# Kernel tuning notes

Hardware: AMD Instinct MI355X
Metric: run time of the kernel (lower is better)

The kernel has to match this reference:

```python
import jax, jax.numpy as jnp
import numpy as np

CHEB_K = 2  # hops per support; stacked terms = 1 + 2*CHEB_K = 5


def setup_inputs() -> dict:
    key = jax.random.key(0)
    k1, k2, k3, k4, k5 = jax.random.split(key, 5)
    B, N, C, O, D = 16, 1024, 64, 64, 10
    return {
        "x": jax.random.normal(k1, (B, N, C), dtype=jnp.float32),
        "adj": jax.random.uniform(k2, (2, B, N, N), dtype=jnp.float32),
        "node_embedding": jax.random.normal(k3, (N, D), dtype=jnp.float32),
        "weights_pool": jax.random.normal(k4, (D, 2 * CHEB_K + 1, C, O), dtype=jnp.float32) * 0.1,
        "bias_pool": jax.random.normal(k5, (D, O), dtype=jnp.float32) * 0.1,
    }


def reference(x, adj, node_embedding, weights_pool, bias_pool):
    # k-hop graph aggregation over each of the 2 supports
    out = [x]
    for s in range(adj.shape[0]):
        a = adj[s]  # [B, N, N]
        x1 = x
        for _ in range(CHEB_K):
            x1 = jnp.einsum('bnm,bmc->bnc', a, x1)
            out.append(x1)
    x_g = jnp.stack(out, axis=2)  # [B, N, K, C] with K = 2*cheb_k+1 (already node-major)
    # per-node hypernetwork weights and bias from node embeddings
    weights = jnp.einsum('nd,dkio->nkio', node_embedding, weights_pool)  # [N, K, C, O]
    bias = node_embedding @ bias_pool  # [N, O]
    # per-node contraction over (K, C)
    return jnp.einsum('bnki,nkio->bno', x_g, weights) + bias
```

## Files before the change

### kernel.cpp

```cpp
#include <hip/hip_runtime.h>
#include <stdint.h>


typedef __attribute__((ext_vector_type(4))) float f32x4;
typedef __attribute__((ext_vector_type(2))) float f32x2;
typedef __attribute__((ext_vector_type(8))) short s16x8;
typedef __attribute__((ext_vector_type(8))) __bf16 bf16x8;

__device__ __forceinline__ unsigned short f2bf(float f) {
  union { float f; uint32_t u; } v; v.f = f;
  uint32_t r = v.u + 0x7FFFu + ((v.u >> 16) & 1u);
  return (unsigned short)(r >> 16);
}
__device__ __forceinline__ uint32_t pack2(float a, float b) {
  return (uint32_t)f2bf(a) | ((uint32_t)f2bf(b) << 16);
}

union FragU { s16x8 s; bf16x8 b; uint32_t u[4]; };

__device__ __forceinline__ void async_cp16(const void* g, void* l) {
  __builtin_amdgcn_global_load_lds(
      (const __attribute__((address_space(1))) void*)g,
      (__attribute__((address_space(3))) void*)l, 16, 0, 0);
}

__global__ __launch_bounds__(256) void prep(const float* __restrict__ x,
                                            const float* __restrict__ wp,
                                            unsigned short* __restrict__ XT0,
                                            unsigned short* __restrict__ wpTb) {
  __shared__ __align__(16) char smem[17160];
  const int tid = threadIdx.x;
  const int bid = blockIdx.x;
  if (bid < 256) {
    unsigned short (*tl)[72] = (unsigned short(*)[72])smem;
    const int b = bid >> 4, n0 = (bid & 15) * 64;
    {
      const int c4 = (tid & 15) * 4;
#pragma unroll
      for (int i = 0; i < 4; ++i) {
        const int row = (tid >> 4) + i * 16;
        f32x4 v =
            *(const f32x4*)(x + ((size_t)(b * 1024 + n0 + row)) * 64 + c4);
        *(uint32_t*)&tl[row][c4]     = pack2(v[0], v[1]);
        *(uint32_t*)&tl[row][c4 + 2] = pack2(v[2], v[3]);
      }
    }
    __syncthreads();
    {
      const int c = tid >> 2;
      const int nch = (tid & 3) * 16;
      s16x8 s0, s1;
#pragma unroll
      for (int j = 0; j < 8; ++j) {
        s0[j] = (short)tl[nch + j][c];
        s1[j] = (short)tl[nch + 8 + j][c];
      }
      unsigned short* p = XT0 + (size_t)(b * 64 + c) * 1024 + n0 + nch;
      *(s16x8*)p = s0;
      *(s16x8*)(p + 8) = s1;
    }
  } else {
    float (*tl)[65] = (float(*)[65])smem;
    const int jj = bid - 256;
    const int d = jj / 5, ki0 = (jj % 5) * 64;
    const float* src = wp + (size_t)d * 20480;
    {
      const int o4 = (tid & 15) * 4;
#pragma unroll
      for (int i = 0; i < 4; ++i) {
        const int row = (tid >> 4) + i * 16;
        f32x4 v = *(const f32x4*)(src + (size_t)(ki0 + row) * 64 + o4);
        tl[row][o4] = v[0]; tl[row][o4 + 1] = v[1];
        tl[row][o4 + 2] = v[2]; tl[row][o4 + 3] = v[3];
      }
    }
    __syncthreads();
    {
      const int o = tid >> 2;
      const int kch = (tid & 3) * 16;
      unsigned short* dst =
          wpTb + (size_t)d * 20480 + (size_t)o * 320 + ki0 + kch;
      s16x8 s0, s1;
#pragma unroll
      for (int j = 0; j < 8; ++j) {
        s0[j] = (short)f2bf(tl[kch + j][o]);
        s1[j] = (short)f2bf(tl[kch + 8 + j][o]);
      }
      *(s16x8*)dst = s0;
      *(s16x8*)(dst + 8) = s1;
    }
  }
}

__device__ __forceinline__ void hop_body(
    char* smem, const float* __restrict__ A,
    const unsigned short* __restrict__ XT, unsigned short* __restrict__ Xoutb,
    unsigned short* __restrict__ XTout, int write_xt, int rowbase) {
  const int tid = threadIdx.x;
  const int wave = tid >> 6, lane = tid & 63;
  const int l15 = lane & 15, q = lane >> 4;

  float* const Ast = (float*)smem;
  unsigned short* const Bst = (unsigned short*)(smem + 32768);

  const float* asrc[4];
  int aldso[4];
#pragma unroll
  for (int i = 0; i < 4; ++i) {
    const int r = wave * 16 + i * 4 + (lane >> 4);
    const int gch = (lane & 15) ^ (r & 7);
    asrc[i] = A + (size_t)(rowbase + r) * 1024 + gch * 4;
    aldso[i] = (wave * 16 + i * 4) * 64;
  }
  const unsigned short* bsrc[2];
  int bldso[2];
#pragma unroll
  for (int i = 0; i < 2; ++i) {
    const int r = wave * 16 + i * 8 + (lane >> 3);
    bsrc[i] = XT + (size_t)r * 1024 + ((lane & 7) ^ (r & 7)) * 8;
    bldso[i] = (wave * 16 + i * 8) * 64;
  }

  f32x4 acc[4];
#pragma unroll
  for (int t = 0; t < 4; ++t) acc[t] = (f32x4){0.f, 0.f, 0.f, 0.f};

  auto issue = [&](int s, int k0) {
#pragma unroll
    for (int i = 0; i < 4; ++i)
      async_cp16(asrc[i] + k0, Ast + s * 4096 + aldso[i]);
#pragma unroll
    for (int i = 0; i < 2; ++i)
      async_cp16(bsrc[i] + k0, Bst + s * 4096 + bldso[i]);
  };
  const int sw = l15 & 7;
  auto compute = [&](int s) {
    const float* Ab = Ast + s * 4096 + (wave * 16 + l15) * 64;
    const unsigned short* Bb = Bst + s * 4096 + l15 * 64;
#pragma unroll
    for (int h = 0; h < 2; ++h) {
      const int g0 = h * 8 + q * 2;
      f32x4 lo = *(const f32x4*)(Ab + (g0 ^ sw) * 4);
      f32x4 hi = *(const f32x4*)(Ab + ((g0 + 1) ^ sw) * 4);
      FragU af;
      af.u[0] = pack2(lo[0], lo[1]);
      af.u[1] = pack2(lo[2], lo[3]);
      af.u[2] = pack2(hi[0], hi[1]);
      af.u[3] = pack2(hi[2], hi[3]);
      const int cko = ((h * 4 + q) ^ sw) * 8;
#pragma unroll
      for (int t = 0; t < 4; ++t) {
        FragU bf;
        bf.s = *(const s16x8*)(Bb + t * 1024 + cko);
        acc[t] = __builtin_amdgcn_mfma_f32_16x16x32_bf16(af.b, bf.b, acc[t],
                                                         0, 0, 0);
      }
    }
  };

  issue(0, 0);
#pragma unroll 1
  for (int kt = 0; kt < 16; ++kt) {
    const int cur = kt & 1;
    __syncthreads();
    if (kt + 1 < 16) issue(cur ^ 1, (kt + 1) * 64);
    compute(cur);
  }

  __syncthreads();
  float (*tile)[65] = (float(*)[65])smem;
#pragma unroll
  for (int t = 0; t < 4; ++t)
#pragma unroll
    for (int rr = 0; rr < 4; ++rr)
      tile[wave * 16 + q * 4 + rr][t * 16 + l15] = acc[t][rr];
  __syncthreads();

  {
    const int row = tid >> 2;
    const int cb = (tid & 3) * 16;
    unsigned short* __restrict__ outp =
        Xoutb + (size_t)(rowbase + row) * 64 + cb;
    s16x8 s0, s1;
#pragma unroll
    for (int j = 0; j < 8; ++j) {
      s0[j] = (short)f2bf(tile[row][cb + j]);
      s1[j] = (short)f2bf(tile[row][cb + 8 + j]);
    }
    *(s16x8*)outp = s0;
    *(s16x8*)(outp + 8) = s1;
  }
  if (write_xt) {
    const int c = tid >> 2;
    const int nch = (tid & 3) * 16;
    unsigned short* __restrict__ xtp = XTout + (size_t)c * 1024 + rowbase + nch;
    s16x8 s0, s1;
#pragma unroll
    for (int j = 0; j < 8; ++j) {
      s0[j] = (short)f2bf(tile[nch + j][c]);
      s1[j] = (short)f2bf(tile[nch + 8 + j][c]);
    }
    *(s16x8*)xtp = s0;
    *(s16x8*)(xtp + 8) = s1;
  }
}

__global__ __launch_bounds__(256, 3) void hop1_kernel(
    const float* __restrict__ adj, const unsigned short* __restrict__ XT0,
    unsigned short* __restrict__ X1b, unsigned short* __restrict__ XT1) {
  __shared__ __align__(16) char smem[49152];
  const int bx = blockIdx.x, slice = blockIdx.y, b = slice & 15;
  hop_body(smem, adj + (size_t)slice * 1048576, XT0 + (size_t)b * 65536,
           X1b + (size_t)slice * 65536, XT1 + (size_t)slice * 65536, 1,
           bx * 64);
}

__global__ __launch_bounds__(256, 3) void hop2_kernel(
    const float* __restrict__ adj, const unsigned short* __restrict__ XT1,
    unsigned short* __restrict__ X2b) {
  __shared__ __align__(16) char smem[49152];
  const int bx = 15 - (int)blockIdx.x;
  const int slice = 31 - (int)blockIdx.y;
  hop_body(smem, adj + (size_t)slice * 1048576, XT1 + (size_t)slice * 65536,
           X2b + (size_t)slice * 65536, (unsigned short*)0, 0, bx * 64);
}

__global__ __launch_bounds__(256, 2) void final_kernel(
    const float* __restrict__ x, const unsigned short* __restrict__ X1b,
    const unsigned short* __restrict__ X2b,
    const unsigned short* __restrict__ wpTb, const float* __restrict__ emb,
    const float* __restrict__ bias_pool, float* __restrict__ out) {
  __shared__ unsigned short xg[2][16][328];
  const int tid = threadIdx.x;
  const int node_base = blockIdx.x * 2;

  for (int u = tid; u < 5120; u += 256) {
    const int nd = u / 2560;
    int rem = u - nd * 2560;
    const int bb = rem / 160;
    const int kiu = rem - bb * 160;
    const int ki = kiu * 2;
    const int k = ki >> 6;
    const int c = ki & 63;
    const int nn = node_base + nd;
    uint32_t w;
    if (k == 0) {
      f32x2 v = *(const f32x2*)(x + ((size_t)bb * 1024 + nn) * 64 + c);
      w = pack2(v[0], v[1]);
    } else {
      const unsigned short* arr = (k == 1 || k == 3) ? X1b : X2b;
      const int s = (k >= 3) ? 1 : 0;
      w = *(const uint32_t*)(arr + ((size_t)(s * 16 + bb) * 1024 + nn) * 64 + c);
    }
    *(uint32_t*)&xg[nd][bb][ki] = w;
  }
  __syncthreads();

  const int wave = tid >> 6, lane = tid & 63;
  const int nd = wave >> 1, oh = wave & 1;
  const int l15 = lane & 15, q = lane >> 4;
  const int n = node_base + nd;

  FragU af[10];
#pragma unroll
  for (int ks = 0; ks < 10; ++ks)
    af[ks].s = *(const s16x8*)&xg[nd][l15][ks * 32 + q * 8];

  f32x4 acc[2];
  acc[0] = (f32x4){0.f, 0.f, 0.f, 0.f};
  acc[1] = (f32x4){0.f, 0.f, 0.f, 0.f};

  const unsigned short* wb0 = wpTb + (size_t)(oh * 32 + l15) * 320 + q * 8;
#pragma unroll 1
  for (int d = 0; d < 10; ++d) {
    const unsigned short* wd = wb0 + (size_t)d * 20480;
    f32x4 tmp[2];
    tmp[0] = (f32x4){0.f, 0.f, 0.f, 0.f};
    tmp[1] = (f32x4){0.f, 0.f, 0.f, 0.f};
#pragma unroll
    for (int ks = 0; ks < 10; ++ks) {
#pragma unroll
      for (int tt = 0; tt < 2; ++tt) {
        FragU bf;
        bf.s = *(const s16x8*)(wd + tt * 5120 + ks * 32);
        tmp[tt] = __builtin_amdgcn_mfma_f32_16x16x32_bf16(af[ks].b, bf.b,
                                                          tmp[tt], 0, 0, 0);
      }
    }
    const float e = emb[n * 10 + d];
#pragma unroll
    for (int tt = 0; tt < 2; ++tt)
#pragma unroll
      for (int rr = 0; rr < 4; ++rr)
        acc[tt][rr] += e * tmp[tt][rr];
  }

#pragma unroll
  for (int tt = 0; tt < 2; ++tt) {
    const int o = (oh * 2 + tt) * 16 + l15;
    float bv = 0.f;
#pragma unroll
    for (int d = 0; d < 10; ++d)
      bv += emb[n * 10 + d] * bias_pool[d * 64 + o];
#pragma unroll
    for (int rr = 0; rr < 4; ++rr) {
      const int bb = q * 4 + rr;
      out[((size_t)bb * 1024 + n) * 64 + o] = acc[tt][rr] + bv;
    }
  }
}

extern "C" void kernel_launch(void* const* d_in, const int* in_sizes, int n_in,
                              void* d_out, int out_size, void* d_ws,
                              size_t ws_size, hipStream_t stream) {
  const float* x   = (const float*)d_in[0];
  const float* adj = (const float*)d_in[1];
  const float* emb = (const float*)d_in[2];
  const float* wp  = (const float*)d_in[3];
  const float* bp  = (const float*)d_in[4];
  float* out = (float*)d_out;

  char* ws = (char*)d_ws;
  unsigned short* XT0  = (unsigned short*)(ws);
  unsigned short* XT1  = (unsigned short*)(ws + ((size_t)2 << 20));
  unsigned short* X1b  = (unsigned short*)(ws + ((size_t)6 << 20));
  unsigned short* X2b  = (unsigned short*)(ws + ((size_t)10 << 20));
  unsigned short* wpTb = (unsigned short*)(ws + ((size_t)14 << 20));

  prep<<<dim3(306), dim3(256), 0, stream>>>(x, wp, XT0, wpTb);
  hop1_kernel<<<dim3(16, 32), dim3(256), 0, stream>>>(adj, XT0, X1b, XT1);
  hop2_kernel<<<dim3(16, 32), dim3(256), 0, stream>>>(adj, XT1, X2b);
  final_kernel<<<dim3(512), dim3(256), 0, stream>>>(x, X1b, X2b, wpTb, emb,
                                                    bp, out);
}
```

Measured before the change: 290.9 us.

## Pre-convert adjacency to bf16 and triple-buffer the hop GEMM pipeline

Adds a conversion pass that writes the fp32 adjacency to a bf16 workspace copy, so both hop kernels load half the bytes and skip the per-tile fp32-to-bf16 packing in the inner loop. The hop main loop moves from double to triple buffering, with explicit vmcnt waits and barriers, and occupancy hint drops to 2 blocks per SM. x is also pre-packed to bf16 for the final kernel. The cost is an extra full read of adj plus a 64MB write before the hops, which could offset the savings if the hops were bandwidth-bound.

```diff
diff --git a/kernel.cpp b/kernel.cpp
--- a/kernel.cpp
+++ b/kernel.cpp
@@ -24,16 +24,35 @@
       (__attribute__((address_space(3))) void*)l, 16, 0, 0);
 }
 
-__global__ __launch_bounds__(256) void prep(const float* __restrict__ x,
-                                            const float* __restrict__ wp,
-                                            unsigned short* __restrict__ XT0,
-                                            unsigned short* __restrict__ wpTb) {
+__global__ __launch_bounds__(256) void cvtprep(
+    const float* __restrict__ adj, unsigned short* __restrict__ adjb,
+    const float* __restrict__ x, const float* __restrict__ wp,
+    unsigned short* __restrict__ XT0, unsigned short* __restrict__ X0b,
+    unsigned short* __restrict__ wpTb) {
   __shared__ __align__(16) char smem[17160];
   const int tid = threadIdx.x;
   const int bid = blockIdx.x;
-  if (bid < 256) {
+
+  if (bid < 8192) {
+    const size_t stride = (size_t)8192 * 256 * 8;
+    for (size_t p = ((size_t)bid * 256 + tid) * 8; p < 33554432u;
+         p += stride) {
+      f32x4 a = *(const f32x4*)(adj + p);
+      f32x4 b = *(const f32x4*)(adj + p + 4);
+      union { s16x8 s; uint32_t u[4]; } o;
+      o.u[0] = pack2(a[0], a[1]);
+      o.u[1] = pack2(a[2], a[3]);
+      o.u[2] = pack2(b[0], b[1]);
+      o.u[3] = pack2(b[2], b[3]);
+      *(s16x8*)(adjb + p) = o.s;
+    }
+    return;
+  }
+
+  const int pid = bid - 8192;
+  if (pid < 256) {
     unsigned short (*tl)[72] = (unsigned short(*)[72])smem;
-    const int b = bid >> 4, n0 = (bid & 15) * 64;
+    const int b = pid >> 4, n0 = (pid & 15) * 64;
     {
       const int c4 = (tid & 15) * 4;
 #pragma unroll
@@ -41,8 +60,12 @@
         const int row = (tid >> 4) + i * 16;
         f32x4 v =
             *(const f32x4*)(x + ((size_t)(b * 1024 + n0 + row)) * 64 + c4);
-        *(uint32_t*)&tl[row][c4]     = pack2(v[0], v[1]);
-        *(uint32_t*)&tl[row][c4 + 2] = pack2(v[2], v[3]);
+        const uint32_t w0 = pack2(v[0], v[1]);
+        const uint32_t w1 = pack2(v[2], v[3]);
+        *(uint32_t*)&tl[row][c4]     = w0;
+        *(uint32_t*)&tl[row][c4 + 2] = w1;
+        const uint64_t wq = (uint64_t)w0 | ((uint64_t)w1 << 32);
+        *(uint64_t*)(X0b + ((size_t)(b * 1024 + n0 + row)) * 64 + c4) = wq;
       }
     }
     __syncthreads();
@@ -61,7 +84,7 @@
     }
   } else {
     float (*tl)[65] = (float(*)[65])smem;
-    const int jj = bid - 256;
+    const int jj = pid - 256;
     const int d = jj / 5, ki0 = (jj % 5) * 64;
     const float* src = wp + (size_t)d * 20480;
     {
@@ -93,32 +116,27 @@
 }
 
 __device__ __forceinline__ void hop_body(
-    char* smem, const float* __restrict__ A,
+    char* smem, const unsigned short* __restrict__ A,
     const unsigned short* __restrict__ XT, unsigned short* __restrict__ Xoutb,
     unsigned short* __restrict__ XTout, int write_xt, int rowbase) {
   const int tid = threadIdx.x;
   const int wave = tid >> 6, lane = tid & 63;
   const int l15 = lane & 15, q = lane >> 4;
 
-  float* const Ast = (float*)smem;
-  unsigned short* const Bst = (unsigned short*)(smem + 32768);
-
-  const float* asrc[4];
-  int aldso[4];
-#pragma unroll
-  for (int i = 0; i < 4; ++i) {
-    const int r = wave * 16 + i * 4 + (lane >> 4);
-    const int gch = (lane & 15) ^ (r & 7);
-    asrc[i] = A + (size_t)(rowbase + r) * 1024 + gch * 4;
-    aldso[i] = (wave * 16 + i * 4) * 64;
-  }
+  unsigned short* const Ast = (unsigned short*)smem;
+  unsigned short* const Bst = (unsigned short*)smem + 12288;
+
+  const int sub = lane >> 3;
+  const int ch = lane & 7;
+  const unsigned short* asrc[2];
   const unsigned short* bsrc[2];
-  int bldso[2];
+  int ldso[2];
 #pragma unroll
   for (int i = 0; i < 2; ++i) {
-    const int r = wave * 16 + i * 8 + (lane >> 3);
-    bsrc[i] = XT + (size_t)r * 1024 + ((lane & 7) ^ (r & 7)) * 8;
-    bldso[i] = (wave * 16 + i * 8) * 64;
+    const int r = wave * 16 + i * 8 + sub;
+    asrc[i] = A + (size_t)(rowbase + r) * 1024 + (ch ^ (r & 7)) * 8;
+    bsrc[i] = XT + (size_t)r * 1024 + (ch ^ (r & 7)) * 8;
+    ldso[i] = (wave * 16 + i * 8) * 64;
   }
 
   f32x4 acc[4];
@@ -127,27 +145,20 @@
 
   auto issue = [&](int s, int k0) {
 #pragma unroll
-    for (int i = 0; i < 4; ++i)
-      async_cp16(asrc[i] + k0, Ast + s * 4096 + aldso[i]);
-#pragma unroll
-    for (int i = 0; i < 2; ++i)
-      async_cp16(bsrc[i] + k0, Bst + s * 4096 + bldso[i]);
+    for (int i = 0; i < 2; ++i) {
+      async_cp16(asrc[i] + k0, Ast + s * 4096 + ldso[i]);
+      async_cp16(bsrc[i] + k0, Bst + s * 4096 + ldso[i]);
+    }
   };
   const int sw = l15 & 7;
   auto compute = [&](int s) {
-    const float* Ab = Ast + s * 4096 + (wave * 16 + l15) * 64;
+    const unsigned short* Ab = Ast + s * 4096 + (wave * 16 + l15) * 64;
     const unsigned short* Bb = Bst + s * 4096 + l15 * 64;
 #pragma unroll
     for (int h = 0; h < 2; ++h) {
-      const int g0 = h * 8 + q * 2;
-      f32x4 lo = *(const f32x4*)(Ab + (g0 ^ sw) * 4);
-      f32x4 hi = *(const f32x4*)(Ab + ((g0 + 1) ^ sw) * 4);
+      const int cko = ((h * 4 + q) ^ sw) * 8;
       FragU af;
-      af.u[0] = pack2(lo[0], lo[1]);
-      af.u[1] = pack2(lo[2], lo[3]);
-      af.u[2] = pack2(hi[0], hi[1]);
-      af.u[3] = pack2(hi[2], hi[3]);
-      const int cko = ((h * 4 + q) ^ sw) * 8;
+      af.s = *(const s16x8*)(Ab + cko);
 #pragma unroll
       for (int t = 0; t < 4; ++t) {
         FragU bf;
@@ -159,13 +170,21 @@
   };
 
   issue(0, 0);
+  issue(1, 64);
 #pragma unroll 1
-  for (int kt = 0; kt < 16; ++kt) {
-    const int cur = kt & 1;
-    __syncthreads();
-    if (kt + 1 < 16) issue(cur ^ 1, (kt + 1) * 64);
-    compute(cur);
-  }
+  for (int kt = 0; kt < 15; ++kt) {
+    asm volatile("s_waitcnt vmcnt(4)" ::: "memory");
+    __builtin_amdgcn_sched_barrier(0);
+    __builtin_amdgcn_s_barrier();
+    __builtin_amdgcn_sched_barrier(0);
+    if (kt < 14) issue((kt + 2) % 3, (kt + 2) * 64);
+    compute(kt % 3);
+  }
+  asm volatile("s_waitcnt vmcnt(0)" ::: "memory");
+  __builtin_amdgcn_sched_barrier(0);
+  __builtin_amdgcn_s_barrier();
+  __builtin_amdgcn_sched_barrier(0);
+  compute(0);
 
   __syncthreads();
   float (*tile)[65] = (float(*)[65])smem;
@@ -205,28 +224,30 @@
   }
 }
 
-__global__ __launch_bounds__(256, 3) void hop1_kernel(
-    const float* __restrict__ adj, const unsigned short* __restrict__ XT0,
-    unsigned short* __restrict__ X1b, unsigned short* __restrict__ XT1) {
+__global__ __launch_bounds__(256, 2) void hop1_kernel(
+    const unsigned short* __restrict__ adjb,
+    const unsigned short* __restrict__ XT0, unsigned short* __restrict__ X1b,
+    unsigned short* __restrict__ XT1) {
   __shared__ __align__(16) char smem[49152];
   const int bx = blockIdx.x, slice = blockIdx.y, b = slice & 15;
-  hop_body(smem, adj + (size_t)slice * 1048576, XT0 + (size_t)b * 65536,
+  hop_body(smem, adjb + (size_t)slice * 1048576, XT0 + (size_t)b * 65536,
            X1b + (size_t)slice * 65536, XT1 + (size_t)slice * 65536, 1,
            bx * 64);
 }
 
-__global__ __launch_bounds__(256, 3) void hop2_kernel(
-    const float* __restrict__ adj, const unsigned short* __restrict__ XT1,
-    unsigned short* __restrict__ X2b) {
+__global__ __launch_bounds__(256, 2) void hop2_kernel(
+    const unsigned short* __restrict__ adjb,
+    const unsigned short* __restrict__ XT1, unsigned short* __restrict__ X2b) {
   __shared__ __align__(16) char smem[49152];
   const int bx = 15 - (int)blockIdx.x;
   const int slice = 31 - (int)blockIdx.y;
-  hop_body(smem, adj + (size_t)slice * 1048576, XT1 + (size_t)slice * 65536,
+  hop_body(smem, adjb + (size_t)slice * 1048576, XT1 + (size_t)slice * 65536,
            X2b + (size_t)slice * 65536, (unsigned short*)0, 0, bx * 64);
 }
 
 __global__ __launch_bounds__(256, 2) void final_kernel(
-    const float* __restrict__ x, const unsigned short* __restrict__ X1b,
+    const unsigned short* __restrict__ X0b,
+    const unsigned short* __restrict__ X1b,
     const unsigned short* __restrict__ X2b,
     const unsigned short* __restrict__ wpTb, const float* __restrict__ emb,
     const float* __restrict__ bias_pool, float* __restrict__ out) {
@@ -243,15 +264,13 @@
     const int k = ki >> 6;
     const int c = ki & 63;
     const int nn = node_base + nd;
-    uint32_t w;
-    if (k == 0) {
-      f32x2 v = *(const f32x2*)(x + ((size_t)bb * 1024 + nn) * 64 + c);
-      w = pack2(v[0], v[1]);
-    } else {
-      const unsigned short* arr = (k == 1 || k == 3) ? X1b : X2b;
-      const int s = (k >= 3) ? 1 : 0;
-      w = *(const uint32_t*)(arr + ((size_t)(s * 16 + bb) * 1024 + nn) * 64 + c);
-    }
+    const unsigned short* base =
+        k == 0 ? X0b
+        : k == 1 ? X1b
+        : k == 2 ? X2b
+        : k == 3 ? X1b + 1048576 : X2b + 1048576;
+    const uint32_t w =
+        *(const uint32_t*)(base + ((size_t)bb * 1024 + nn) * 64 + c);
     *(uint32_t*)&xg[nd][bb][ki] = w;
   }
   __syncthreads();
@@ -321,15 +340,18 @@
   float* out = (float*)d_out;
 
   char* ws = (char*)d_ws;
-  unsigned short* XT0  = (unsigned short*)(ws);
-  unsigned short* XT1  = (unsigned short*)(ws + ((size_t)2 << 20));
-  unsigned short* X1b  = (unsigned short*)(ws + ((size_t)6 << 20));
-  unsigned short* X2b  = (unsigned short*)(ws + ((size_t)10 << 20));
-  unsigned short* wpTb = (unsigned short*)(ws + ((size_t)14 << 20));
-
-  prep<<<dim3(306), dim3(256), 0, stream>>>(x, wp, XT0, wpTb);
-  hop1_kernel<<<dim3(16, 32), dim3(256), 0, stream>>>(adj, XT0, X1b, XT1);
-  hop2_kernel<<<dim3(16, 32), dim3(256), 0, stream>>>(adj, XT1, X2b);
-  final_kernel<<<dim3(512), dim3(256), 0, stream>>>(x, X1b, X2b, wpTb, emb,
+  unsigned short* adjb = (unsigned short*)(ws);
+  unsigned short* XT0  = (unsigned short*)(ws + ((size_t)68 << 20));
+  unsigned short* XT1  = (unsigned short*)(ws + ((size_t)70 << 20));
+  unsigned short* X0b  = (unsigned short*)(ws + ((size_t)74 << 20));
+  unsigned short* X1b  = (unsigned short*)(ws + ((size_t)76 << 20));
+  unsigned short* X2b  = (unsigned short*)(ws + ((size_t)80 << 20));
+  unsigned short* wpTb = (unsigned short*)(ws + ((size_t)84 << 20));
+
+  cvtprep<<<dim3(8498), dim3(256), 0, stream>>>(adj, adjb, x, wp, XT0, X0b,
+                                                wpTb);
+  hop1_kernel<<<dim3(16, 32), dim3(256), 0, stream>>>(adjb, XT0, X1b, XT1);
+  hop2_kernel<<<dim3(16, 32), dim3(256), 0, stream>>>(adjb, XT1, X2b);
+  final_kernel<<<dim3(512), dim3(256), 0, stream>>>(X0b, X1b, X2b, wpTb, emb,
                                                     bp, out);
 }
```

After: 290.6 us. About the same (-0.1%).
